# Kernel optimization log

Hardware: AMD Instinct MI355X
Metric: run time of the kernel (lower is better)

Reference implementation:

```python
import jax, jax.numpy as jnp
import numpy as np

N_HEADS = 16

def setup_inputs() -> dict:
    key = jax.random.key(0)
    ks = jax.random.split(key, 5)
    d = 2048
    s = 0.02
    return {
        "x": jax.random.normal(ks[0], (1, 2048, d), dtype=jnp.float32),
        "Wq": jax.random.normal(ks[1], (d, d), dtype=jnp.float32) * s,
        "bq": jnp.zeros((d,), jnp.float32),
        "Wk": jax.random.normal(ks[2], (d, d), dtype=jnp.float32) * s,
        "bk": jnp.zeros((d,), jnp.float32),
        "Wv": jax.random.normal(ks[3], (d, d), dtype=jnp.float32) * s,
        "bv": jnp.zeros((d,), jnp.float32),
        "Wo": jax.random.normal(ks[4], (d, d), dtype=jnp.float32) * s,
        "bo": jnp.zeros((d,), jnp.float32),
    }

def reference(x, Wq, bq, Wk, bk, Wv, bv, Wo, bo):
    B, S, D = x.shape
    H = N_HEADS
    dk = D // H
    # QKV projections -> [B, H, S, dk]
    def proj(W, b):
        return (x @ W + b).reshape(B, S, H, dk).transpose(0, 2, 1, 3)
    q, k, v = proj(Wq, bq), proj(Wk, bk), proj(Wv, bv)
    scores = jnp.einsum('bhqd,bhkd->bhqk', q, k) / jnp.sqrt(jnp.float32(dk))
    # _apply_sliding_window_attention: block-reshaped tril == plain causal mask
    causal = jnp.tril(jnp.ones((S, S), dtype=bool))
    scores = jnp.where(causal, scores, -jnp.inf)
    probs = jax.nn.softmax(scores, axis=-1)
    out = jnp.einsum('bhqk,bhkd->bhqd', probs, v)  # [B,H,S,dk]
    out = out.transpose(0, 2, 1, 3).reshape(B, S, D)
    return out @ Wo + bo
```

## Files before the change

### kernel.cpp

```cpp
#include <hip/hip_runtime.h>
#include <hip/hip_bf16.h>
#include <stdint.h>

typedef unsigned short u16;
typedef __attribute__((ext_vector_type(8))) __bf16 bf16x8;
typedef __attribute__((ext_vector_type(4))) float f32x4;

#define LOG2E 1.4426950408889634f

__device__ __forceinline__ float bf2f(u16 u) {
  union { uint32_t u; float f; } v; v.u = ((uint32_t)u) << 16;
  return v.f;
}

__device__ __forceinline__ uint32_t pk2(float a, float b) {
  union { __hip_bfloat162 h; uint32_t u; } x;
  x.h = __float22bfloat162_rn(make_float2(a, b));
  return x.u;
}

__device__ __forceinline__ void gl_lds16(const void* g, void* l) {
  __builtin_amdgcn_global_load_lds((const __attribute__((address_space(1))) void*)g,
                                   (__attribute__((address_space(3))) void*)l,
                                   16, 0, 0);
}

__device__ __forceinline__ f32x4 mfma16(bf16x8 a, bf16x8 b, f32x4 c) {
  return __builtin_amdgcn_mfma_f32_16x16x32_bf16(a, b, c, 0, 0, 0);
}

__device__ __forceinline__ void bar() {
  asm volatile("" ::: "memory");
  __builtin_amdgcn_s_barrier();
  asm volatile("" ::: "memory");
}

__global__ void cvt_bf16(const float* __restrict__ src, u16* __restrict__ dst) {
  int i = (blockIdx.x * 256 + threadIdx.x) * 4;
  float4 f = *(const float4*)(src + i);
  uint2 o;
  o.x = pk2(f.x, f.y);
  o.y = pk2(f.z, f.w);
  *(uint2*)(dst + i) = o;
}

__global__ void transpose_cvt(const float* __restrict__ W0, const float* __restrict__ W1,
                              const float* __restrict__ W2, const float* __restrict__ W3,
                              u16* __restrict__ out) {
  __shared__ float tile[64][65];
  int z = blockIdx.z;
  const float* W = (z == 0) ? W0 : (z == 1) ? W1 : (z == 2) ? W2 : W3;
  u16* dst = out + (size_t)z * 2048 * 2048;
  int k0 = blockIdx.y * 64, n0 = blockIdx.x * 64;
  int lx = threadIdx.x & 63, ly = threadIdx.x >> 6;
#pragma unroll
  for (int p = 0; p < 16; ++p) {
    int row = p * 4 + ly;
    tile[row][lx] = W[(size_t)(k0 + row) * 2048 + n0 + lx];
  }
  __syncthreads();
  int kc = threadIdx.x & 7;
  int rbase = threadIdx.x >> 3;
#pragma unroll
  for (int p = 0; p < 2; ++p) {
    int n = rbase + p * 32;
    uint4 o;
    o.x = pk2(tile[kc * 8 + 0][n], tile[kc * 8 + 1][n]);
    o.y = pk2(tile[kc * 8 + 2][n], tile[kc * 8 + 3][n]);
    o.z = pk2(tile[kc * 8 + 4][n], tile[kc * 8 + 5][n]);
    o.w = pk2(tile[kc * 8 + 6][n], tile[kc * 8 + 7][n]);
    *(uint4*)(dst + (size_t)(n0 + n) * 2048 + k0 + kc * 8) = o;
  }
}

__launch_bounds__(256, 2)
__global__ void gemm_bt(const u16* __restrict__ A, const u16* __restrict__ Bt,
                        const float* __restrict__ b0, const float* __restrict__ b1,
                        const float* __restrict__ b2,
                        u16* __restrict__ outQ, u16* __restrict__ outK,
                        u16* __restrict__ outVT) {
  extern __shared__ char smem[];
  u16* As = (u16*)smem;
  u16* Bs = (u16*)(smem + 16384);
  const int K = 2048;
  const int tid = threadIdx.x;
  const int lane = tid & 63, wid = tid >> 6;
  const int c = lane & 15, q = lane >> 4;
  const int wm = wid >> 1, wn = wid & 1;
  const int tm = blockIdx.y, tn = blockIdx.x;
  const size_t Abase = (size_t)tm * 128 * K;
  const size_t Bbase = (size_t)tn * 128 * K;

  f32x4 acc[4][4] = {};

  for (int kt = 0; kt < K / 64; ++kt) {
#pragma unroll
    for (int t = 0; t < 4; ++t) {
      int slot = wid * 256 + t * 64 + lane;
      int row = slot >> 3, cs = slot & 7;
      int cc = cs ^ (row & 7);
      const u16* ga = A + Abase + (size_t)row * K + kt * 64 + cc * 8;
      gl_lds16(ga, (char*)As + (size_t)(wid * 256 + t * 64) * 16);
      const u16* gb = Bt + Bbase + (size_t)row * K + kt * 64 + cc * 8;
      gl_lds16(gb, (char*)Bs + (size_t)(wid * 256 + t * 64) * 16);
    }
    __syncthreads();
#pragma unroll
    for (int kc = 0; kc < 2; ++kc) {
      bf16x8 af[4], bfr[4];
#pragma unroll
      for (int i = 0; i < 4; ++i) {
        int rowa = wm * 64 + i * 16 + c;
        int cha = ((kc << 2) | q) ^ (rowa & 7);
        af[i] = *(const bf16x8*)((const char*)As + rowa * 128 + cha * 16);
        int rowb = wn * 64 + i * 16 + c;
        int chb = ((kc << 2) | q) ^ (rowb & 7);
        bfr[i] = *(const bf16x8*)((const char*)Bs + rowb * 128 + chb * 16);
      }
#pragma unroll
      for (int i = 0; i < 4; ++i)
#pragma unroll
        for (int j = 0; j < 4; ++j)
          acc[i][j] = mfma16(af[i], bfr[j], acc[i][j]);
    }
    __syncthreads();
  }

  int proj = tn >> 4;
  int h = tn & 15;
  const float* bias = (proj == 0) ? b0 : (proj == 1) ? b1 : b2;
  if (proj < 2) {
    u16* out = (proj == 0) ? outQ : outK;
    float scale = (proj == 0) ? 0.08838834764831845f : 1.0f;
#pragma unroll
    for (int i = 0; i < 4; ++i) {
      int s0 = tm * 128 + wm * 64 + i * 16 + q * 4;
#pragma unroll
      for (int j = 0; j < 4; ++j) {
        int d = wn * 64 + j * 16 + c;
        float bv = bias[h * 128 + d];
        uint32_t p01 = pk2((acc[i][j][0] + bv) * scale, (acc[i][j][1] + bv) * scale);
        uint32_t p23 = pk2((acc[i][j][2] + bv) * scale, (acc[i][j][3] + bv) * scale);
        u16* o = out + ((size_t)h * 2048 + s0) * 128 + d;
        o[0]   = (u16)p01;
        o[128] = (u16)(p01 >> 16);
        o[256] = (u16)p23;
        o[384] = (u16)(p23 >> 16);
      }
    }
  } else {
    u16* Cs = (u16*)smem;
#pragma unroll
    for (int i = 0; i < 4; ++i) {
      int sl = wm * 64 + i * 16 + q * 4;
#pragma unroll
      for (int j = 0; j < 4; ++j) {
        int dl = wn * 64 + j * 16 + c;
        float bv = bias[h * 128 + dl];
        uint2 pk;
        pk.x = pk2(acc[i][j][0] + bv, acc[i][j][1] + bv);
        pk.y = pk2(acc[i][j][2] + bv, acc[i][j][3] + bv);
        *(uint2*)(Cs + dl * 136 + sl) = pk;
      }
    }
    __syncthreads();
#pragma unroll
    for (int rr = 0; rr < 8; ++rr) {
      int d = rr * 16 + (tid >> 4);
      int sc = (tid & 15) * 8;
      uint4 vv = *(const uint4*)(Cs + d * 136 + sc);
      *(uint4*)(outVT + ((size_t)(h * 128 + d)) * 2048 + tm * 128 + sc) = vv;
    }
  }
}

__launch_bounds__(256, 2)
__global__ void gemm_op(const u16* __restrict__ A, const u16* __restrict__ Bt,
                        const float* __restrict__ bias, float* __restrict__ out) {
  extern __shared__ char smem[];
  u16* As = (u16*)smem;
  u16* Bs = (u16*)(smem + 16384);
  const int K = 2048;
  const int tid = threadIdx.x;
  const int lane = tid & 63, wid = tid >> 6;
  const int c = lane & 15, q = lane >> 4;
  const int wm = wid >> 1, wn = wid & 1;
  const int tm = blockIdx.y, tn = blockIdx.x;
  const size_t Abase = (size_t)tm * 128 * K;
  const size_t Bbase = (size_t)tn * 64 * K;

  f32x4 acc[4][2] = {};

  for (int kt = 0; kt < K / 64; ++kt) {
#pragma unroll
    for (int t = 0; t < 4; ++t) {
      int slot = wid * 256 + t * 64 + lane;
      int row = slot >> 3, cs = slot & 7;
      int cc = cs ^ (row & 7);
      gl_lds16(A + Abase + (size_t)row * K + kt * 64 + cc * 8,
               (char*)As + (size_t)(wid * 256 + t * 64) * 16);
    }
#pragma unroll
    for (int t = 0; t < 2; ++t) {
      int slot = wid * 128 + t * 64 + lane;
      int row = slot >> 3, cs = slot & 7;
      int cc = cs ^ (row & 7);
      gl_lds16(Bt + Bbase + (size_t)row * K + kt * 64 + cc * 8,
               (char*)Bs + (size_t)(wid * 128 + t * 64) * 16);
    }
    __syncthreads();
#pragma unroll
    for (int kc = 0; kc < 2; ++kc) {
      bf16x8 af[4], bfr[2];
#pragma unroll
      for (int i = 0; i < 4; ++i) {
        int rowa = wm * 64 + i * 16 + c;
        int cha = ((kc << 2) | q) ^ (rowa & 7);
        af[i] = *(const bf16x8*)((const char*)As + rowa * 128 + cha * 16);
      }
#pragma unroll
      for (int j = 0; j < 2; ++j) {
        int rowb = wn * 32 + j * 16 + c;
        int chb = ((kc << 2) | q) ^ (rowb & 7);
        bfr[j] = *(const bf16x8*)((const char*)Bs + rowb * 128 + chb * 16);
      }
#pragma unroll
      for (int i = 0; i < 4; ++i)
#pragma unroll
        for (int j = 0; j < 2; ++j)
          acc[i][j] = mfma16(af[i], bfr[j], acc[i][j]);
    }
    __syncthreads();
  }

#pragma unroll
  for (int i = 0; i < 4; ++i) {
    int rowg = tm * 128 + wm * 64 + i * 16 + q * 4;
#pragma unroll
    for (int j = 0; j < 2; ++j) {
      int colg = tn * 64 + wn * 32 + j * 16 + c;
      float bv = bias[colg];
#pragma unroll
      for (int r = 0; r < 4; ++r)
        out[(size_t)(rowg + r) * 2048 + colg] = acc[i][j][r] + bv;
    }
  }
}

__launch_bounds__(256, 2)
__global__ void attn_kernel(const u16* __restrict__ Qb, const u16* __restrict__ Kb,
                            const u16* __restrict__ Vt,
                            u16* __restrict__ Opb, float* __restrict__ lpb) {
  extern __shared__ char smem[];
  int b = blockIdx.x;
  int split, qt, h;
  if (b < 256) { split = 0; qt = b >> 4; h = b & 15; }
  else { split = 1; int idx = b - 256; qt = 15 - (idx >> 4); h = idx & 15; }
  u16* Op = Opb + (size_t)split * 4194304;
  float* lp = lpb + (size_t)split * 32768;
  const int ktBase = split ? (qt + 1) : 0;
  const int ntiles = qt + 1;

  const int tid = threadIdx.x, lane = tid & 63, wid = tid >> 6;
  const int c = lane & 15, q = lane >> 4;

  bf16x8 qf[2][4];
#pragma unroll
  for (int i = 0; i < 2; ++i) {
    int s = qt * 128 + wid * 32 + i * 16 + c;
    const u16* qrow = Qb + ((size_t)h * 2048 + s) * 128;
#pragma unroll
    for (int kc = 0; kc < 4; ++kc)
      qf[i][kc] = *(const bf16x8*)(qrow + kc * 32 + q * 8);
  }

  f32x4 oacc[2][8] = {};
  float lst[2][4] = {};

  auto STAGE = [&](int kt, int buf) {
    char* Kd = smem + buf * 32768;
    char* Vd = smem + buf * 32768 + 16384;
#pragma unroll
    for (int t = 0; t < 4; ++t) {
      int slot = (wid * 4 + t) * 64 + lane;
      int rowk = slot >> 4, csk = slot & 15;
      int cck = csk ^ (rowk & 7);
      const u16* gk = Kb + ((size_t)h * 2048 + kt * 64 + rowk) * 128 + cck * 8;
      gl_lds16(gk, Kd + (size_t)((wid * 4 + t) * 64) * 16);
      int rowv = slot >> 3, csv = slot & 7;
      int ccv = csv ^ (rowv & 7);
      const u16* gv = Vt + ((size_t)(h * 128 + rowv)) * 2048 + kt * 64 + ccv * 8;
      gl_lds16(gv, Vd + (size_t)((wid * 4 + t) * 64) * 16);
    }
  };

  STAGE(ktBase, 0);
  int cur = 0;

  for (int tt = 0; tt < ntiles; ++tt) {
    const int kt = ktBase + tt;
    if (tt + 1 < ntiles) {
      STAGE(kt + 1, cur ^ 1);
      __builtin_amdgcn_sched_barrier(0);
      asm volatile("s_waitcnt vmcnt(8)" ::: "memory");
    } else {
      asm volatile("s_waitcnt vmcnt(0)" ::: "memory");
    }
    __builtin_amdgcn_sched_barrier(0);
    bar();

    const char* Ksb = smem + cur * 32768;
    const char* Vsb = smem + cur * 32768 + 16384;

    f32x4 sacc[2][4] = {};
    __builtin_amdgcn_s_setprio(1);
#pragma unroll
    for (int kc = 0; kc < 4; ++kc) {
      bf16x8 bfr[4];
#pragma unroll
      for (int j = 0; j < 4; ++j) {
        int row = j * 16 + c;
        int ch = ((kc << 2) | q) ^ (row & 7);
        bfr[j] = *(const bf16x8*)(Ksb + row * 256 + ch * 16);
      }
#pragma unroll
      for (int i = 0; i < 2; ++i)
#pragma unroll
        for (int j = 0; j < 4; ++j)
          sacc[i][j] = mfma16(qf[i][kc], bfr[j], sacc[i][j]);
    }
    __builtin_amdgcn_s_setprio(0);
    bar();

    if (kt >= 2 * qt) {
#pragma unroll
      for (int i = 0; i < 2; ++i)
#pragma unroll
        for (int j = 0; j < 4; ++j) {
          int key = kt * 64 + j * 16 + c;
#pragma unroll
          for (int r = 0; r < 4; ++r) {
            int qrow = qt * 128 + wid * 32 + i * 16 + q * 4 + r;
            if (key > qrow) sacc[i][j][r] = -1e30f;
          }
        }
    }

#pragma unroll
    for (int i = 0; i < 2; ++i)
#pragma unroll
      for (int j = 0; j < 4; ++j)
#pragma unroll
        for (int r = 0; r < 4; ++r) {
          float p = __builtin_amdgcn_exp2f(sacc[i][j][r] * LOG2E);
          sacc[i][j][r] = p;
          lst[i][r] += p;
        }

    char* Pw = smem + cur * 32768 + wid * 4096;
#pragma unroll
    for (int i = 0; i < 2; ++i)
#pragma unroll
      for (int j = 0; j < 4; ++j) {
        uint32_t p01 = pk2(sacc[i][j][0], sacc[i][j][1]);
        uint32_t p23 = pk2(sacc[i][j][2], sacc[i][j][3]);
        int cb = (j << 1) | (c >> 3);
        int r0 = i * 16 + q * 4;
        int wb = (c & 7) << 1;
        *(u16*)(Pw + (r0 + 0) * 128 + ((cb ^ ((r0 + 0) & 7)) << 4) + wb) = (u16)p01;
        *(u16*)(Pw + (r0 + 1) * 128 + ((cb ^ ((r0 + 1) & 7)) << 4) + wb) = (u16)(p01 >> 16);
        *(u16*)(Pw + (r0 + 2) * 128 + ((cb ^ ((r0 + 2) & 7)) << 4) + wb) = (u16)p23;
        *(u16*)(Pw + (r0 + 3) * 128 + ((cb ^ ((r0 + 3) & 7)) << 4) + wb) = (u16)(p23 >> 16);
      }

    __builtin_amdgcn_s_setprio(1);
#pragma unroll
    for (int kc = 0; kc < 2; ++kc) {
      bf16x8 af[2], bv[8];
#pragma unroll
      for (int i = 0; i < 2; ++i) {
        int prow = i * 16 + c;
        af[i] = *(const bf16x8*)(Pw + prow * 128 + ((((kc << 2) | q) ^ (prow & 7)) << 4));
      }
#pragma unroll
      for (int jo = 0; jo < 8; ++jo) {
        int row = jo * 16 + c;
        int ch = ((kc << 2) | q) ^ (row & 7);
        bv[jo] = *(const bf16x8*)(Vsb + row * 128 + ch * 16);
      }
#pragma unroll
      for (int i = 0; i < 2; ++i)
#pragma unroll
        for (int jo = 0; jo < 8; ++jo)
          oacc[i][jo] = mfma16(bv[jo], af[i], oacc[i][jo]);
    }
    __builtin_amdgcn_s_setprio(0);
    bar();
    cur ^= 1;
  }

#pragma unroll
  for (int i = 0; i < 2; ++i)
#pragma unroll
    for (int r = 0; r < 4; ++r) {
      float l = lst[i][r];
      l += __shfl_xor(l, 1);
      l += __shfl_xor(l, 2);
      l += __shfl_xor(l, 4);
      l += __shfl_xor(l, 8);
      if (c == 0)
        lp[(size_t)h * 2048 + qt * 128 + wid * 32 + i * 16 + q * 4 + r] = l;
    }
#pragma unroll
  for (int i = 0; i < 2; ++i) {
    int s = qt * 128 + wid * 32 + i * 16 + c;
#pragma unroll
    for (int jo = 0; jo < 8; ++jo) {
      uint2 o;
      o.x = pk2(oacc[i][jo][0], oacc[i][jo][1]);
      o.y = pk2(oacc[i][jo][2], oacc[i][jo][3]);
      *(uint2*)(Op + ((size_t)h * 2048 + s) * 128 + jo * 16 + q * 4) = o;
    }
  }
}

__global__ void attn_combine(const u16* __restrict__ Opb, const float* __restrict__ lpb,
                             u16* __restrict__ AO) {
  int g = blockIdx.x * 256 + threadIdx.x;
  int row = g >> 4;
  int dd = (g & 15) * 8;
  int h = row >> 11, s = row & 2047;
  float inv = 1.0f / (lpb[row] + lpb[row + 32768]);
  uint4 a = *(const uint4*)(Opb + (size_t)row * 128 + dd);
  uint4 bb = *(const uint4*)(Opb + 4194304 + (size_t)row * 128 + dd);
  const u16* pa = (const u16*)&a;
  const u16* pb = (const u16*)&bb;
  uint4 res;
  uint32_t* pr = (uint32_t*)&res;
#pragma unroll
  for (int t = 0; t < 4; ++t)
    pr[t] = pk2((bf2f(pa[2 * t]) + bf2f(pb[2 * t])) * inv,
                (bf2f(pa[2 * t + 1]) + bf2f(pb[2 * t + 1])) * inv);
  *(uint4*)(AO + (size_t)s * 2048 + h * 128 + dd) = res;
}

extern "C" void kernel_launch(void* const* d_in, const int* in_sizes, int n_in,
                              void* d_out, int out_size, void* d_ws, size_t ws_size,
                              hipStream_t stream) {
  const float* x  = (const float*)d_in[0];
  const float* Wq = (const float*)d_in[1];
  const float* bq = (const float*)d_in[2];
  const float* Wk = (const float*)d_in[3];
  const float* bk = (const float*)d_in[4];
  const float* Wv = (const float*)d_in[5];
  const float* bv = (const float*)d_in[6];
  const float* Wo = (const float*)d_in[7];
  const float* bo = (const float*)d_in[8];

  char* ws = (char*)d_ws;
  u16* xb = (u16*)(ws);
  u16* wt = (u16*)(ws + (size_t)8  * 1048576);
  u16* Qb = (u16*)(ws + (size_t)40 * 1048576);
  u16* Kb = (u16*)(ws + (size_t)48 * 1048576);
  u16* Vt = (u16*)(ws + (size_t)56 * 1048576);
  u16* AO = (u16*)(ws + (size_t)64 * 1048576);
  u16* Opb = (u16*)(ws);
  float* lpb = (float*)d_out;

  cvt_bf16<<<4096, 256, 0, stream>>>(x, xb);
  transpose_cvt<<<dim3(32, 32, 4), 256, 0, stream>>>(Wq, Wk, Wv, Wo, wt);
  gemm_bt<<<dim3(48, 16), 256, 34816, stream>>>(xb, wt, bq, bk, bv, Qb, Kb, Vt);
  attn_kernel<<<512, 256, 65536, stream>>>(Qb, Kb, Vt, Opb, lpb);
  attn_combine<<<2048, 256, 0, stream>>>(Opb, lpb, AO);
  gemm_op<<<dim3(32, 16), 256, 24576, stream>>>(AO, wt + (size_t)3 * 2048 * 2048,
                                                bo, (float*)d_out);
}
```

Baseline: 256.9 us.

## Rewrite QKV GEMM with 256x256 tiles, double-buffered LDS and swizzled block order

Replaces the 128x128-tile QKV projection GEMM with a 512-thread kernel that computes 256x256 tiles. It double-buffers 128KB of LDS, prefetching the next k-tile in quarter phases with partial vmcnt waits, raises wave priority around the MFMA bursts, and remaps block IDs so neighbouring blocks share operands. The goal is more operand reuse per load and overlap of global loads with matrix math. In exchange it uses large LDS and many registers, launches only 192 blocks on a 256-CU device, and makes the V-transpose epilogue run in two halves.

```diff
diff --git a/kernel.cpp b/kernel.cpp
--- a/kernel.cpp
+++ b/kernel.cpp
@@ -73,74 +73,97 @@
   }
 }
 
-__launch_bounds__(256, 2)
-__global__ void gemm_bt(const u16* __restrict__ A, const u16* __restrict__ Bt,
-                        const float* __restrict__ b0, const float* __restrict__ b1,
-                        const float* __restrict__ b2,
-                        u16* __restrict__ outQ, u16* __restrict__ outK,
-                        u16* __restrict__ outVT) {
+__launch_bounds__(512, 2)
+__global__ void gemm_qkv(const u16* __restrict__ A, const u16* __restrict__ Bt,
+                         const float* __restrict__ b0, const float* __restrict__ b1,
+                         const float* __restrict__ b2,
+                         u16* __restrict__ outQ, u16* __restrict__ outK,
+                         u16* __restrict__ outVT) {
   extern __shared__ char smem[];
-  u16* As = (u16*)smem;
-  u16* Bs = (u16*)(smem + 16384);
-  const int K = 2048;
+  const int K = 2048, NT = 32;
   const int tid = threadIdx.x;
   const int lane = tid & 63, wid = tid >> 6;
   const int c = lane & 15, q = lane >> 4;
-  const int wm = wid >> 1, wn = wid & 1;
-  const int tm = blockIdx.y, tn = blockIdx.x;
-  const size_t Abase = (size_t)tm * 128 * K;
-  const size_t Bbase = (size_t)tn * 128 * K;
-
-  f32x4 acc[4][4] = {};
-
-  for (int kt = 0; kt < K / 64; ++kt) {
-#pragma unroll
-    for (int t = 0; t < 4; ++t) {
-      int slot = wid * 256 + t * 64 + lane;
-      int row = slot >> 3, cs = slot & 7;
-      int cc = cs ^ (row & 7);
-      const u16* ga = A + Abase + (size_t)row * K + kt * 64 + cc * 8;
-      gl_lds16(ga, (char*)As + (size_t)(wid * 256 + t * 64) * 16);
-      const u16* gb = Bt + Bbase + (size_t)row * K + kt * 64 + cc * 8;
-      gl_lds16(gb, (char*)Bs + (size_t)(wid * 256 + t * 64) * 16);
-    }
-    __syncthreads();
-#pragma unroll
-    for (int kc = 0; kc < 2; ++kc) {
-      bf16x8 af[4], bfr[4];
-#pragma unroll
-      for (int i = 0; i < 4; ++i) {
-        int rowa = wm * 64 + i * 16 + c;
-        int cha = ((kc << 2) | q) ^ (rowa & 7);
-        af[i] = *(const bf16x8*)((const char*)As + rowa * 128 + cha * 16);
-        int rowb = wn * 64 + i * 16 + c;
-        int chb = ((kc << 2) | q) ^ (rowb & 7);
-        bfr[i] = *(const bf16x8*)((const char*)Bs + rowb * 128 + chb * 16);
-      }
-#pragma unroll
-      for (int i = 0; i < 4; ++i)
-#pragma unroll
-        for (int j = 0; j < 4; ++j)
-          acc[i][j] = mfma16(af[i], bfr[j], acc[i][j]);
-    }
-    __syncthreads();
-  }
-
-  int proj = tn >> 4;
-  int h = tn & 15;
-  const float* bias = (proj == 0) ? b0 : (proj == 1) ? b1 : b2;
+  const int wm = wid >> 2, wn = wid & 3;
+  int raw = blockIdx.x;
+  int sbid = (raw & 7) * 24 + (raw >> 3);
+  const int tm = sbid / 24, tn = sbid % 24;
+  const size_t Abase = (size_t)tm * 256 * K;
+  const size_t Bbase = (size_t)tn * 256 * K;
+
+  f32x4 acc[8][4] = {};
+
+  auto STAGE = [&](int t2, int u) {
+    char* dst = smem + (t2 & 1) * 65536 + u * 16384;
+    const u16* src = (u & 1) ? (Bt + Bbase) : (A + Abase);
+    int kh = u >> 1;
+#pragma unroll
+    for (int l = 0; l < 2; ++l) {
+      int s = l * 512 + wid * 64 + lane;
+      int r = s >> 2;
+      int qq = (s & 3) ^ (r & 3);
+      gl_lds16(src + (size_t)r * K + t2 * 64 + kh * 32 + qq * 8, dst + (size_t)s * 16);
+    }
+  };
+
+#define QKV_PHASE(P)                                                              \
+  {                                                                               \
+    if (t == NT - 1 && (P) >= 2) { asm volatile("s_waitcnt vmcnt(0)" ::: "memory"); } \
+    else                         { asm volatile("s_waitcnt vmcnt(4)" ::: "memory"); } \
+    bar();                                                                        \
+    if (t + 1 < NT) STAGE(t + 1, (P));                                            \
+    const int kcP = (P) >> 1, nhP = (P) & 1;                                      \
+    const char* Ab = smem + buf * 65536 + (kcP * 2) * 16384;                      \
+    const char* Bb = smem + buf * 65536 + (kcP * 2 + 1) * 16384;                  \
+    if (nhP == 0) {                                                               \
+      _Pragma("unroll") for (int mi = 0; mi < 8; ++mi) {                          \
+        int row = wm * 128 + mi * 16 + c;                                         \
+        af[mi] = *(const bf16x8*)(Ab + row * 64 + ((q ^ (row & 3)) << 4));        \
+      }                                                                           \
+    }                                                                             \
+    bf16x8 bfv[2];                                                                \
+    _Pragma("unroll") for (int jj = 0; jj < 2; ++jj) {                            \
+      int row = wn * 64 + (nhP * 2 + jj) * 16 + c;                                \
+      bfv[jj] = *(const bf16x8*)(Bb + row * 64 + ((q ^ (row & 3)) << 4));         \
+    }                                                                             \
+    __builtin_amdgcn_s_setprio(1);                                                \
+    _Pragma("unroll") for (int mi = 0; mi < 8; ++mi) {                            \
+      acc[mi][nhP * 2 + 0] = mfma16(af[mi], bfv[0], acc[mi][nhP * 2 + 0]);        \
+      acc[mi][nhP * 2 + 1] = mfma16(af[mi], bfv[1], acc[mi][nhP * 2 + 1]);        \
+    }                                                                             \
+    __builtin_amdgcn_s_setprio(0);                                                \
+  }
+
+#pragma unroll
+  for (int u = 0; u < 4; ++u) STAGE(0, u);
+
+#pragma unroll 2
+  for (int t = 0; t < NT; ++t) {
+    const int buf = t & 1;
+    bf16x8 af[8];
+    QKV_PHASE(0)
+    QKV_PHASE(1)
+    QKV_PHASE(2)
+    QKV_PHASE(3)
+  }
+#undef QKV_PHASE
+
+  const int proj = tn >> 3;
+  const int tnp = tn & 7;
   if (proj < 2) {
     u16* out = (proj == 0) ? outQ : outK;
-    float scale = (proj == 0) ? 0.08838834764831845f : 1.0f;
-#pragma unroll
-    for (int i = 0; i < 4; ++i) {
-      int s0 = tm * 128 + wm * 64 + i * 16 + q * 4;
-#pragma unroll
-      for (int j = 0; j < 4; ++j) {
-        int d = wn * 64 + j * 16 + c;
-        float bv = bias[h * 128 + d];
-        uint32_t p01 = pk2((acc[i][j][0] + bv) * scale, (acc[i][j][1] + bv) * scale);
-        uint32_t p23 = pk2((acc[i][j][2] + bv) * scale, (acc[i][j][3] + bv) * scale);
+    const float* bias = (proj == 0) ? b0 : b1;
+    const float scale = (proj == 0) ? 0.08838834764831845f : 1.0f;
+#pragma unroll
+    for (int mi = 0; mi < 8; ++mi) {
+      int s0 = tm * 256 + wm * 128 + mi * 16 + q * 4;
+#pragma unroll
+      for (int ni = 0; ni < 4; ++ni) {
+        int colp = tnp * 256 + wn * 64 + ni * 16 + c;
+        int h = colp >> 7, d = colp & 127;
+        float bv = bias[colp];
+        uint32_t p01 = pk2((acc[mi][ni][0] + bv) * scale, (acc[mi][ni][1] + bv) * scale);
+        uint32_t p23 = pk2((acc[mi][ni][2] + bv) * scale, (acc[mi][ni][3] + bv) * scale);
         u16* o = out + ((size_t)h * 2048 + s0) * 128 + d;
         o[0]   = (u16)p01;
         o[128] = (u16)(p01 >> 16);
@@ -151,25 +174,31 @@
   } else {
     u16* Cs = (u16*)smem;
 #pragma unroll
-    for (int i = 0; i < 4; ++i) {
-      int sl = wm * 64 + i * 16 + q * 4;
-#pragma unroll
-      for (int j = 0; j < 4; ++j) {
-        int dl = wn * 64 + j * 16 + c;
-        float bv = bias[h * 128 + dl];
-        uint2 pk;
-        pk.x = pk2(acc[i][j][0] + bv, acc[i][j][1] + bv);
-        pk.y = pk2(acc[i][j][2] + bv, acc[i][j][3] + bv);
-        *(uint2*)(Cs + dl * 136 + sl) = pk;
-      }
-    }
-    __syncthreads();
-#pragma unroll
-    for (int rr = 0; rr < 8; ++rr) {
-      int d = rr * 16 + (tid >> 4);
-      int sc = (tid & 15) * 8;
-      uint4 vv = *(const uint4*)(Cs + d * 136 + sc);
-      *(uint4*)(outVT + ((size_t)(h * 128 + d)) * 2048 + tm * 128 + sc) = vv;
+    for (int hh = 0; hh < 2; ++hh) {
+      bar();
+      if ((wn >> 1) == hh) {
+#pragma unroll
+        for (int mi = 0; mi < 8; ++mi) {
+          int sl = wm * 128 + mi * 16 + q * 4;
+#pragma unroll
+          for (int ni = 0; ni < 4; ++ni) {
+            int dl = (wn & 1) * 64 + ni * 16 + c;
+            float bv = b2[tnp * 256 + hh * 128 + dl];
+            uint2 pk;
+            pk.x = pk2(acc[mi][ni][0] + bv, acc[mi][ni][1] + bv);
+            pk.y = pk2(acc[mi][ni][2] + bv, acc[mi][ni][3] + bv);
+            *(uint2*)(Cs + dl * 264 + sl) = pk;
+          }
+        }
+      }
+      bar();
+#pragma unroll
+      for (int kk = 0; kk < 8; ++kk) {
+        int cid = kk * 512 + tid;
+        int d = cid >> 5, sc = (cid & 31) * 8;
+        uint4 vv = *(const uint4*)(Cs + d * 264 + sc);
+        *(uint4*)(outVT + ((size_t)((tnp * 2 + hh) * 128 + d)) * 2048 + tm * 256 + sc) = vv;
+      }
     }
   }
 }
@@ -467,9 +496,16 @@
   u16* Opb = (u16*)(ws);
   float* lpb = (float*)d_out;
 
+  static bool inited = false;
+  if (!inited) {
+    hipFuncSetAttribute((const void*)gemm_qkv,
+                        hipFuncAttributeMaxDynamicSharedMemorySize, 131072);
+    inited = true;
+  }
+
   cvt_bf16<<<4096, 256, 0, stream>>>(x, xb);
   transpose_cvt<<<dim3(32, 32, 4), 256, 0, stream>>>(Wq, Wk, Wv, Wo, wt);
-  gemm_bt<<<dim3(48, 16), 256, 34816, stream>>>(xb, wt, bq, bk, bv, Qb, Kb, Vt);
+  gemm_qkv<<<192, 512, 131072, stream>>>(xb, wt, bq, bk, bv, Qb, Kb, Vt);
   attn_kernel<<<512, 256, 65536, stream>>>(Qb, Kb, Vt, Opb, lpb);
   attn_combine<<<2048, 256, 0, stream>>>(Opb, lpb, AO);
   gemm_op<<<dim3(32, 16), 256, 24576, stream>>>(AO, wt + (size_t)3 * 2048 * 2048,
```

After: 303.7 us. +18.2%, slower.
